# Kernel tuning notes

Measured on AMD Instinct MI355X. Metric: run time of the kernel, lower is better.

The kernel has to match this reference:

```python
import jax, jax.numpy as jnp
import numpy as np

N, C, H, W = 4, 128, 128, 128
G, K, PAD, DIL = 4, 3, 1, 1
P = K * K
HID = 4 * C
EPS = 1e-6


def ln(x, w, b):
    m = jnp.mean(x, -1, keepdims=True)
    v = jnp.mean((x - m) ** 2, -1, keepdims=True)
    return (x - m) * jax.lax.rsqrt(v + EPS) * w + b


def linear(x, w, b):
    return x @ w.T + b


def grid_sample_zeros(img, grid):
    # img: (B,Hi,Wi,Cc); grid: (B,L,P,2) xy in [-1,1]; bilinear, zeros padding, align_corners=False
    B, Hi, Wi, Cc = img.shape
    gx = (grid[..., 0] + 1.0) * (Wi * 0.5) - 0.5
    gy = (grid[..., 1] + 1.0) * (Hi * 0.5) - 0.5
    x0 = jnp.floor(gx)
    y0 = jnp.floor(gy)
    wx1 = gx - x0
    wy1 = gy - y0
    flat = img.reshape(B, Hi * Wi, Cc)
    Bq, L, Pq = gx.shape

    def tap(yy, xx, wgt):
        valid = (xx >= 0) & (xx <= Wi - 1) & (yy >= 0) & (yy <= Hi - 1)
        idx = (jnp.clip(yy, 0, Hi - 1) * Wi + jnp.clip(xx, 0, Wi - 1)).astype(jnp.int32)
        v = jnp.take_along_axis(flat, idx.reshape(B, L * Pq)[..., None], axis=1)
        return v.reshape(B, L, Pq, Cc) * (wgt * valid)[..., None]

    return (tap(y0, x0, (1 - wx1) * (1 - wy1))
            + tap(y0, x0 + 1, wx1 * (1 - wy1))
            + tap(y0 + 1, x0, (1 - wx1) * wy1)
            + tap(y0 + 1, x0 + 1, wx1 * wy1))


def dcn_core(x, offset, mask):
    # faithful port of dcnv3_core_pytorch (stride=1, offset_scale=1.0)
    n, h, w, c = x.shape
    gc = c // G
    xp = jnp.pad(x, ((0, 0), (PAD, PAD), (PAD, PAD), (0, 0)))
    hi, wi = h + 2 * PAD, w + 2 * PAD
    base = (DIL * (K - 1)) // 2 + 0.5
    ref_y = (base + jnp.arange(h, dtype=jnp.float32)) / hi
    ref_x = (base + jnp.arange(w, dtype=jnp.float32)) / wi
    ref = jnp.stack([jnp.broadcast_to(ref_x[None, :], (h, w)),
                     jnp.broadcast_to(ref_y[:, None], (h, w))], -1)  # (h,w,2) xy
    ks = jnp.arange(K, dtype=jnp.float32) * DIL - (DIL * (K - 1)) // 2
    gxk, gyk = jnp.meshgrid(ks, ks, indexing='ij')  # x slow, y fast (torch meshgrid order)
    grid = jnp.tile(jnp.stack([gxk / wi, gyk / hi], -1).reshape(P, 2), (G, 1))  # (G*P,2)
    sn = jnp.array([wi, hi], jnp.float32)
    loc = ref[None, :, :, None, :] + grid[None, None, None] + offset.reshape(n, h, w, G * P, 2) / sn
    sg = (2.0 * loc - 1.0).reshape(n, h * w, G, P, 2).transpose(0, 2, 1, 3, 4).reshape(n * G, h * w, P, 2)
    img = xp.reshape(n, hi, wi, G, gc).transpose(0, 3, 1, 2, 4).reshape(n * G, hi, wi, gc)
    samp = grid_sample_zeros(img, sg)  # (n*G, h*w, P, gc)
    m = mask.reshape(n, h * w, G, P).transpose(0, 2, 1, 3).reshape(n * G, h * w, P)
    out = jnp.einsum('blpc,blp->blc', samp, m)
    return out.reshape(n, G, h * w, gc).transpose(0, 2, 1, 3).reshape(n, h, w, c)


def dcn_forward(xcl, dw_w, dw_b, dwln_w, dwln_b, off_w, off_b, mask_w, mask_b, outproj_w, outproj_b):
    n, h, w, c = xcl.shape
    y = jax.lax.conv_general_dilated(xcl.transpose(0, 3, 1, 2), dw_w, (1, 1),
                                     ((PAD, PAD), (PAD, PAD)),
                                     dimension_numbers=('NCHW', 'OIHW', 'NCHW'),
                                     feature_group_count=C)
    y = y + dw_b[None, :, None, None]
    x1 = jax.nn.gelu(ln(y.transpose(0, 2, 3, 1), dwln_w, dwln_b), approximate=False)
    offset = linear(x1, off_w, off_b)
    m = jax.nn.softmax(linear(x1, mask_w, mask_b).reshape(n, h, w, G, P), -1).reshape(n, h, w, G * P)
    out = dcn_core(x1, offset, m)
    return linear(out, outproj_w, outproj_b)


def setup_inputs():
    key = jax.random.key(0)
    ks = jax.random.split(key, 8)
    s = 0.02
    return {
        "x": jax.random.normal(ks[0], (N, C, H, W), jnp.float32),
        "norm1_w": jnp.ones((C,), jnp.float32), "norm1_b": jnp.zeros((C,), jnp.float32),
        "dw_w": jax.random.normal(ks[1], (C, 1, K, K), jnp.float32) * 0.1,
        "dw_b": jnp.zeros((C,), jnp.float32),
        "dwln_w": jnp.ones((C,), jnp.float32), "dwln_b": jnp.zeros((C,), jnp.float32),
        "off_w": jax.random.normal(ks[2], (G * P * 2, C), jnp.float32) * 0.05,
        "off_b": jax.random.normal(ks[3], (G * P * 2,), jnp.float32) * 0.5,
        "mask_w": jax.random.normal(ks[4], (G * P, C), jnp.float32) * 0.05,
        "mask_b": jnp.zeros((G * P,), jnp.float32),
        "outproj_w": jax.random.normal(ks[5], (C, C), jnp.float32) * s,
        "outproj_b": jnp.zeros((C,), jnp.float32),
        "norm2_w": jnp.ones((C,), jnp.float32), "norm2_b": jnp.zeros((C,), jnp.float32),
        "fc1_w": jax.random.normal(ks[6], (HID, C), jnp.float32) * s,
        "fc1_b": jnp.zeros((HID,), jnp.float32),
        "fc2_w": jax.random.normal(ks[7], (C, HID), jnp.float32) * s,
        "fc2_b": jnp.zeros((C,), jnp.float32),
    }


def reference(x, norm1_w, norm1_b, dw_w, dw_b, dwln_w, dwln_b, off_w, off_b,
              mask_w, mask_b, outproj_w, outproj_b, norm2_w, norm2_b,
              fc1_w, fc1_b, fc2_w, fc2_b):
    # pre-norm branch (layer_scale=None, post_norm=False, res_post_norm=False, drop_path=Identity)
    xcl = ln(x.transpose(0, 2, 3, 1), norm1_w, norm1_b)  # channels_first -> channels_last LN
    d = dcn_forward(xcl, dw_w, dw_b, dwln_w, dwln_b, off_w, off_b, mask_w, mask_b, outproj_w, outproj_b)
    x = x + d.transpose(0, 3, 1, 2)
    y = ln(x.transpose(0, 2, 3, 1), norm2_w, norm2_b)
    y = linear(jax.nn.gelu(linear(y, fc1_w, fc1_b), approximate=False), fc2_w, fc2_b)
    return x + y.transpose(0, 3, 1, 2)
```

## Files before the change

### kernel.cpp

```cpp
#include <hip/hip_runtime.h>

typedef unsigned short ushort_t;
typedef short short8 __attribute__((ext_vector_type(8)));
typedef float f32x4 __attribute__((ext_vector_type(4)));
typedef ushort_t ushort8v __attribute__((ext_vector_type(8)));
typedef ushort_t ushort4v __attribute__((ext_vector_type(4)));

#define HWsz 16384
#define NHWsz 65536
#define YS 136

__device__ __forceinline__ float b2f(ushort_t u){ return __uint_as_float(((unsigned)u)<<16); }
__device__ __forceinline__ ushort_t f2b(float f){
  unsigned x = __float_as_uint(f);
  x += 0x7fffu + ((x>>16)&1u);
  return (ushort_t)(x>>16);
}
__device__ __forceinline__ float gelu_fast(float x){
  float t = x*x;
  float e = __expf(x*(1.5957691216f + 0.0713548163f*t));
  return x - x*__builtin_amdgcn_rcpf(1.0f + e);
}

#define XSW(p, b) ((p)*256 + ((b) ^ (((p)&7)<<4)))

__global__ __launch_bounds__(256) void kW_cvt(const float* __restrict__ w1, const float* __restrict__ w2,
    const float* __restrict__ offw, const float* __restrict__ maskw, const float* __restrict__ dww,
    const float* __restrict__ pw, const float* __restrict__ offb, const float* __restrict__ mb,
    ushort_t* __restrict__ w1b, ushort_t* __restrict__ w2b, ushort_t* __restrict__ owmb,
    float* __restrict__ dwwT, ushort_t* __restrict__ pwh, ushort_t* __restrict__ pwl,
    float* __restrict__ obm){
  int i = blockIdx.x*256 + threadIdx.x;
  w1b[i] = f2b(w1[i]);
  w2b[i] = f2b(w2[i]);
  if (i < 16384){
    int row = i >> 7, k = i & 127;
    float v = 0.f;
    if (row < 72) v = offw[row*128 + k];
    else if (row < 108) v = maskw[(row-72)*128 + k];
    owmb[i] = f2b(v);
    float pv = pw[i];
    ushort_t hi = f2b(pv);
    pwh[i] = hi;
    pwl[i] = f2b(pv - b2f(hi));
  }
  if (i < 1152){
    int k = i >> 7, c = i & 127;
    dwwT[i] = dww[c*9 + k];
  }
  if (i < 128){
    obm[i] = (i < 72) ? offb[i] : ((i < 108) ? mb[i-72] : 0.f);
  }
}

__global__ __launch_bounds__(256) void kA_ln1(const float* __restrict__ x,
    const float* __restrict__ w, const float* __restrict__ b,
    ushort_t* __restrict__ xcl){
  __shared__ float tile[128*66];
  __shared__ float psum[256], psq[256];
  __shared__ float ms[64], rs[64];
  int t = threadIdx.x;
  int pos0 = blockIdx.x * 64;
  int n = pos0 >> 14, hw0 = pos0 & 16383;
  const float* xb = x + (size_t)n*128*HWsz + hw0;
  for (int i=0;i<32;i++){
    int e = i*256+t;
    int c = e>>6, p = e&63;
    tile[c*66+p] = xb[(size_t)c*HWsz + p];
  }
  __syncthreads();
  {
    int part = t>>6, p = t&63;
    float s=0.f, q=0.f;
    for (int c=part*32; c<part*32+32; c++){ float v = tile[c*66+p]; s+=v; q+=v*v; }
    psum[part*64+p]=s; psq[part*64+p]=q;
  }
  __syncthreads();
  if (t<64){
    float s=psum[t]+psum[64+t]+psum[128+t]+psum[192+t];
    float q=psq[t]+psq[64+t]+psq[128+t]+psq[192+t];
    float m = s*(1.0f/128.0f);
    float v = q*(1.0f/128.0f)-m*m;
    ms[t]=m; rs[t]=rsqrtf(v+1e-6f);
  }
  __syncthreads();
  for (int i=0;i<32;i++){
    int e = i*256+t;
    int p = e>>7, c = e&127;
    float v = (tile[c*66+p]-ms[p])*rs[p]*w[c]+b[c];
    xcl[(size_t)(pos0+p)*128 + c] = f2b(v);
  }
}

__global__ __launch_bounds__(256) void kB_dw(const ushort_t* __restrict__ xcl,
    const float* __restrict__ dwwT, const float* __restrict__ dwb,
    const float* __restrict__ lnw, const float* __restrict__ lnb,
    ushort_t* __restrict__ x1){
  __shared__ float partS[16*17], partQ[16*17];
  __shared__ float ms[16], rs[16];
  int t = threadIdx.x;
  int pos0 = blockIdx.x*16;
  int n = pos0>>14, hw0 = pos0&16383, h = hw0>>7, w0 = hw0&127;
  int pp = t>>4, l = t&15, ch0 = l*8;
  int w = w0 + pp;
  float acc[8];
  {
    float4 b0 = *(const float4*)(dwb + ch0);
    float4 b1 = *(const float4*)(dwb + ch0 + 4);
    acc[0]=b0.x; acc[1]=b0.y; acc[2]=b0.z; acc[3]=b0.w;
    acc[4]=b1.x; acc[5]=b1.y; acc[6]=b1.z; acc[7]=b1.w;
  }
  #pragma unroll
  for (int kh=0; kh<3; kh++){
    int hy = h + kh - 1;
    if ((unsigned)hy < 128u){
      #pragma unroll
      for (int kw=0; kw<3; kw++){
        int wx = w + kw - 1;
        if ((unsigned)wx < 128u){
          ushort8v xv = *(const ushort8v*)(xcl + ((size_t)(n*16384 + hy*128 + wx))*128 + ch0);
          const float* wr = dwwT + (kh*3+kw)*128 + ch0;
          float4 w0v = *(const float4*)(wr);
          float4 w1v = *(const float4*)(wr+4);
          acc[0] += b2f(xv[0])*w0v.x; acc[1] += b2f(xv[1])*w0v.y;
          acc[2] += b2f(xv[2])*w0v.z; acc[3] += b2f(xv[3])*w0v.w;
          acc[4] += b2f(xv[4])*w1v.x; acc[5] += b2f(xv[5])*w1v.y;
          acc[6] += b2f(xv[6])*w1v.z; acc[7] += b2f(xv[7])*w1v.w;
        }
      }
    }
  }
  {
    float s=0.f, q=0.f;
    #pragma unroll
    for (int j=0;j<8;j++){ s+=acc[j]; q+=acc[j]*acc[j]; }
    partS[pp*17+l]=s; partQ[pp*17+l]=q;
  }
  __syncthreads();
  {
    int p = t>>4, j = t&15;
    float s = partS[p*17+j];
    float q = partQ[p*17+j];
    s += __shfl_xor(s, 1);  q += __shfl_xor(q, 1);
    s += __shfl_xor(s, 2);  q += __shfl_xor(q, 2);
    s += __shfl_xor(s, 4);  q += __shfl_xor(q, 4);
    s += __shfl_xor(s, 8);  q += __shfl_xor(q, 8);
    if (j == 0){
      float m = s*(1.0f/128.0f);
      float var = q*(1.0f/128.0f) - m*m;
      ms[p]=m; rs[p]=rsqrtf(var+1e-6f);
    }
  }
  __syncthreads();
  {
    float m = ms[pp], r = rs[pp];
    float4 lw0 = *(const float4*)(lnw + ch0);
    float4 lw1 = *(const float4*)(lnw + ch0 + 4);
    float4 lb0 = *(const float4*)(lnb + ch0);
    float4 lb1 = *(const float4*)(lnb + ch0 + 4);
    float lw[8] = {lw0.x,lw0.y,lw0.z,lw0.w,lw1.x,lw1.y,lw1.z,lw1.w};
    float lb[8] = {lb0.x,lb0.y,lb0.z,lb0.w,lb1.x,lb1.y,lb1.z,lb1.w};
    ushort8v o;
    #pragma unroll
    for (int j=0;j<8;j++){
      float v = (acc[j]-m)*r*lw[j]+lb[j];
      o[j] = f2b(gelu_fast(v));
    }
    *(ushort8v*)(x1 + (size_t)(pos0+pp)*128 + ch0) = o;
  }
}

#define RS 120
__global__ __launch_bounds__(256) void kCD_dcn(const ushort_t* __restrict__ x1,
    const ushort_t* __restrict__ owmb, const float* __restrict__ obm,
    ushort_t* __restrict__ dcnout){
  __shared__ __align__(16) ushort_t xLb[16*YS];
  __shared__ float raw[16*RS];
  __shared__ __align__(16) float descW[576*4];
  __shared__ __align__(16) int   descO[576*4];
  int t = threadIdx.x;
  int pos0 = blockIdx.x*16;
  int n = pos0>>14, hw0 = pos0&16383, h = hw0>>7, w0 = hw0&127;
  const size_t imgbase = (size_t)n*16384*128;

  *(ushort8v*)(xLb + (t>>4)*YS + (t&15)*8) = *(const ushort8v*)(x1 + (size_t)pos0*128 + t*8);
  __syncthreads();

  {
    int wave = t>>6, lane = t&63;
    int ma = lane&15, quad = lane>>4;
    short8 afrag[4];
    #pragma unroll
    for (int ks=0; ks<4; ks++)
      afrag[ks] = *(const short8*)(xLb + ma*YS + ks*32 + quad*8);
    f32x4 acc[2];
    acc[0] = (f32x4){0.f,0.f,0.f,0.f};
    acc[1] = (f32x4){0.f,0.f,0.f,0.f};
    #pragma unroll
    for (int tile=0; tile<2; tile++){
      const ushort_t* brow = owmb + (size_t)(wave*32 + tile*16 + ma)*128 + quad*8;
      #pragma unroll
      for (int ks=0; ks<4; ks++){
        short8 bfrag = *(const short8*)(brow + ks*32);
        acc[tile] = __builtin_amdgcn_mfma_f32_16x16x32_bf16(bfrag, afrag[ks], acc[tile], 0,0,0);
      }
    }
    #pragma unroll
    for (int tile=0; tile<2; tile++){
      int row0 = wave*32 + tile*16 + quad*4;
      if (row0 < 112){
        f32x4 bias4 = *(const f32x4*)(obm + row0);
        f32x4 o;
        #pragma unroll
        for (int r=0;r<4;r++) o[r] = acc[tile][r] + bias4[r];
        *(f32x4*)(raw + ma*RS + row0) = o;
      }
    }
  }
  __syncthreads();

  if (t < 64){
    int p = t>>2, g = t&3;
    float* mr = raw + p*RS + 72 + g*9;
    float mx = -1e30f;
    for (int q=0;q<9;q++) mx = fmaxf(mx, mr[q]);
    float e[9]; float ssum=0.f;
    for (int q=0;q<9;q++){ e[q]=expf(mr[q]-mx); ssum+=e[q]; }
    float inv = 1.0f/ssum;
    for (int q=0;q<9;q++) mr[q] = e[q]*inv;
  }
  __syncthreads();

  for (int it=0; it<3; it++){
    int tid = t + 256*it;
    if (tid < 576){
      int pp = tid/36, rem = tid - pp*36;
      int g = rem/9, p = rem - g*9;
      int i = p/3, j = p - i*3;
      float ox = raw[pp*RS + 2*(g*9+p)];
      float oy = raw[pp*RS + 2*(g*9+p)+1];
      float mval = raw[pp*RS + 72 + g*9 + p];
      float px = (float)(w0 + pp + i - 1) + ox;
      float py = (float)(h + j - 1) + oy;
      float fx0 = floorf(px), fy0 = floorf(py);
      int ix0 = (int)fx0, iy0 = (int)fy0;
      float fx = px - fx0, fy = py - fy0;
      float vx0 = ((unsigned)ix0     < 128u) ? 1.f : 0.f;
      float vx1 = ((unsigned)(ix0+1) < 128u) ? 1.f : 0.f;
      float vy0 = ((unsigned)iy0     < 128u) ? 1.f : 0.f;
      float vy1 = ((unsigned)(iy0+1) < 128u) ? 1.f : 0.f;
      int cx0 = min(max(ix0,0),127), cx1 = min(max(ix0+1,0),127);
      int cy0 = min(max(iy0,0),127), cy1 = min(max(iy0+1,0),127);
      float4 wv;
      wv.x = (1.f-fx)*(1.f-fy)*mval*vx0*vy0;
      wv.y = fx*(1.f-fy)*mval*vx1*vy0;
      wv.z = (1.f-fx)*fy*mval*vx0*vy1;
      wv.w = fx*fy*mval*vx1*vy1;
      int4 ov;
      ov.x = (cy0*128+cx0)*128;
      ov.y = (cy0*128+cx1)*128;
      ov.z = (cy1*128+cx0)*128;
      ov.w = (cy1*128+cx1)*128;
      *(float4*)(descW + tid*4) = wv;
      *(int4*)(descO + tid*4) = ov;
    }
  }
  __syncthreads();

  {
    int pp = t>>4, l = t&15;
    int ch0 = l*8, g = l>>2;
    const ushort_t* ib = x1 + imgbase + ch0;
    float acc[8];
    #pragma unroll
    for (int j=0;j<8;j++) acc[j]=0.f;
    int dbase = pp*36 + g*9;
    #pragma unroll
    for (int p=0;p<9;p++){
      float4 wv = *(const float4*)(descW + (dbase+p)*4);
      int4  ov = *(const int4*)(descO + (dbase+p)*4);
      ushort8v v00 = *(const ushort8v*)(ib + ov.x);
      ushort8v v10 = *(const ushort8v*)(ib + ov.y);
      ushort8v v01 = *(const ushort8v*)(ib + ov.z);
      ushort8v v11 = *(const ushort8v*)(ib + ov.w);
      #pragma unroll
      for (int j=0;j<8;j++){
        float s = wv.x*b2f(v00[j]) + wv.y*b2f(v10[j]) + wv.z*b2f(v01[j]) + wv.w*b2f(v11[j]);
        acc[j] += s;
      }
    }
    ushort8v outv;
    #pragma unroll
    for (int j=0;j<8;j++) outv[j] = f2b(acc[j]);
    *(ushort8v*)(dcnout + (size_t)(pos0+pp)*128 + ch0) = outv;
  }
}

__global__ __launch_bounds__(256) void kEFG(const ushort_t* __restrict__ dcnout,
    const ushort_t* __restrict__ pwh, const ushort_t* __restrict__ pwl,
    const float* __restrict__ pb, const float* __restrict__ x,
    const float* __restrict__ n2w, const float* __restrict__ n2b,
    const ushort_t* __restrict__ w1b, const float* __restrict__ b1,
    const ushort_t* __restrict__ w2b, const float* __restrict__ b2,
    float* __restrict__ out){
  __shared__ __align__(16) char dxn[64*256];
  __shared__ __align__(16) char hidb[64*256];
  float* partS = (float*)hidb;
  float* partQ = partS + 64*17;
  float* msh   = partQ + 64*17;
  float* rsh   = msh + 64;

  int t = threadIdx.x;
  int pos0 = blockIdx.x*64;
  int n = pos0>>14, hw0 = pos0&16383;
  int wave = t>>6, lane = t&63;
  int ma = lane&15, quad = lane>>4;

  #pragma unroll
  for (int i=0;i<4;i++){
    int e = i*256 + t;
    int row = e>>4, c16 = e&15;
    ushort8v v = *(const ushort8v*)(dcnout + (size_t)pos0*128 + (size_t)e*8);
    *(ushort8v*)(dxn + XSW(row, c16*16)) = v;
  }
  __syncthreads();

  f32x4 acc[2][4];
  #pragma unroll
  for (int i=0;i<2;i++)
    #pragma unroll
    for (int mt=0; mt<4; mt++) acc[i][mt] = (f32x4){0.f,0.f,0.f,0.f};
  #pragma unroll
  for (int tile=0; tile<2; tile++){
    int c0 = wave*32 + tile*16;
    const ushort_t* bh = pwh + (size_t)(c0 + ma)*128 + quad*8;
    const ushort_t* bl = pwl + (size_t)(c0 + ma)*128 + quad*8;
    short8 bfh[4], bfl[4];
    #pragma unroll
    for (int ks=0; ks<4; ks++){
      bfh[ks] = *(const short8*)(bh + ks*32);
      bfl[ks] = *(const short8*)(bl + ks*32);
    }
    #pragma unroll
    for (int mt=0; mt<4; mt++){
      short8 a[4];
      #pragma unroll
      for (int ks=0; ks<4; ks++)
        a[ks] = *(const short8*)(dxn + XSW(mt*16+ma, ks*64 + quad*16));
      #pragma unroll
      for (int ks=0; ks<4; ks++){
        acc[tile][mt] = __builtin_amdgcn_mfma_f32_16x16x32_bf16(bfh[ks], a[ks], acc[tile][mt], 0,0,0);
        acc[tile][mt] = __builtin_amdgcn_mfma_f32_16x16x32_bf16(bfl[ks], a[ks], acc[tile][mt], 0,0,0);
      }
    }
  }

  ushort4v vbp[2][4];
  float sAcc[4], qAcc[4];
  #pragma unroll
  for (int mt=0; mt<4; mt++){ sAcc[mt]=0.f; qAcc[mt]=0.f; }
  #pragma unroll
  for (int tile=0; tile<2; tile++){
    int c0 = wave*32 + tile*16 + quad*4;
    f32x4 bias4 = *(const f32x4*)(pb + c0);
    #pragma unroll
    for (int mt=0; mt<4; mt++){
      int p = mt*16 + ma;
      ushort4v ov;
      #pragma unroll
      for (int r=0;r<4;r++){
        float res = x[((size_t)(n*128) + c0 + r)*HWsz + hw0 + p];
        float v = acc[tile][mt][r] + bias4[r] + res;
        ushort_t ub = f2b(v);
        ov[r] = ub;
        float vv = b2f(ub);
        sAcc[mt] += vv; qAcc[mt] += vv*vv;
      }
      vbp[tile][mt] = ov;
    }
  }
  #pragma unroll
  for (int mt=0; mt<4; mt++){
    int p = mt*16 + ma;
    partS[p*17 + wave*4 + quad] = sAcc[mt];
    partQ[p*17 + wave*4 + quad] = qAcc[mt];
  }
  __syncthreads();
  {
    int p = t>>2, j = t&3;
    float s = partS[p*17+4*j] + partS[p*17+4*j+1] + partS[p*17+4*j+2] + partS[p*17+4*j+3];
    float q = partQ[p*17+4*j] + partQ[p*17+4*j+1] + partQ[p*17+4*j+2] + partQ[p*17+4*j+3];
    s += __shfl_xor(s, 1);  q += __shfl_xor(q, 1);
    s += __shfl_xor(s, 2);  q += __shfl_xor(q, 2);
    if (j == 0){
      float m = s*(1.0f/128.0f);
      float var = q*(1.0f/128.0f) - m*m;
      msh[p] = m; rsh[p] = rsqrtf(var+1e-6f);
    }
  }
  __syncthreads();

  #pragma unroll
  for (int tile=0; tile<2; tile++){
    int c0 = wave*32 + tile*16 + quad*4;
    f32x4 w4 = *(const f32x4*)(n2w + c0);
    f32x4 b4 = *(const f32x4*)(n2b + c0);
    #pragma unroll
    for (int mt=0; mt<4; mt++){
      int p = mt*16 + ma;
      float m = msh[p], r = rsh[p];
      ushort4v nv;
      #pragma unroll
      for (int rr=0;rr<4;rr++) nv[rr] = f2b((b2f(vbp[tile][mt][rr])-m)*r*w4[rr] + b4[rr]);
      *(ushort4v*)(dxn + XSW(p, c0*2)) = nv;
    }
  }
  __syncthreads();

  f32x4 acc2[2][4];
  #pragma unroll
  for (int i=0;i<2;i++)
    #pragma unroll
    for (int mt=0; mt<4; mt++) acc2[i][mt] = (f32x4){0.f,0.f,0.f,0.f};

  #pragma unroll
  for (int nc=0; nc<4; nc++){
    #pragma unroll
    for (int tt=0; tt<2; tt++){
      int n0g = nc*128 + wave*32 + tt*16;
      const ushort_t* brow = w1b + (size_t)(n0g + ma)*128 + quad*8;
      short8 bf[4];
      #pragma unroll
      for (int ks=0; ks<4; ks++) bf[ks] = *(const short8*)(brow + ks*32);
      int n0 = n0g + quad*4;
      f32x4 bias4 = *(const f32x4*)(b1 + n0);
      int nloc = wave*32 + tt*16 + quad*4;
      #pragma unroll
      for (int mt=0; mt<4; mt++){
        short8 a[4];
        #pragma unroll
        for (int ks=0; ks<4; ks++)
          a[ks] = *(const short8*)(dxn + XSW(mt*16+ma, ks*64 + quad*16));
        f32x4 a0 = (f32x4){0.f,0.f,0.f,0.f};
        #pragma unroll
        for (int ks=0; ks<4; ks++)
          a0 = __builtin_amdgcn_mfma_f32_16x16x32_bf16(bf[ks], a[ks], a0, 0,0,0);
        ushort4v hv;
        #pragma unroll
        for (int r=0;r<4;r++) hv[r] = f2b(gelu_fast(a0[r] + bias4[r]));
        *(ushort4v*)(hidb + XSW(mt*16+ma, nloc*2)) = hv;
      }
    }
    __syncthreads();

    #pragma unroll
    for (int ksl=0; ksl<4; ksl++){
      int kk = nc*128 + ksl*32;
      short8 wc0 = *(const short8*)(w2b + (size_t)(wave*32 + ma)*512 + kk + quad*8);
      short8 wc1 = *(const short8*)(w2b + (size_t)(wave*32 + 16 + ma)*512 + kk + quad*8);
      #pragma unroll
      for (int mt=0; mt<4; mt++){
        short8 hc = *(const short8*)(hidb + XSW(mt*16+ma, ksl*64 + quad*16));
        acc2[0][mt] = __builtin_amdgcn_mfma_f32_16x16x32_bf16(wc0, hc, acc2[0][mt], 0,0,0);
        acc2[1][mt] = __builtin_amdgcn_mfma_f32_16x16x32_bf16(wc1, hc, acc2[1][mt], 0,0,0);
      }
    }
    if (nc < 3) __syncthreads();
  }

  #pragma unroll
  for (int tile=0; tile<2; tile++){
    int c0 = wave*32 + tile*16 + quad*4;
    f32x4 bias4 = *(const f32x4*)(b2 + c0);
    #pragma unroll
    for (int mt=0; mt<4; mt++){
      int p = mt*16 + ma;
      #pragma unroll
      for (int r=0;r<4;r++){
        float v = acc2[tile][mt][r] + bias4[r] + b2f(vbp[tile][mt][r]);
        out[((size_t)(n*128) + c0 + r)*HWsz + hw0 + p] = v;
      }
    }
  }
}

extern "C" void kernel_launch(void* const* d_in, const int* in_sizes, int n_in,
                              void* d_out, int out_size, void* d_ws, size_t ws_size,
                              hipStream_t stream){
  const float* x     = (const float*)d_in[0];
  const float* n1w   = (const float*)d_in[1];
  const float* n1b   = (const float*)d_in[2];
  const float* dww   = (const float*)d_in[3];
  const float* dwb   = (const float*)d_in[4];
  const float* dwlnw = (const float*)d_in[5];
  const float* dwlnb = (const float*)d_in[6];
  const float* offw  = (const float*)d_in[7];
  const float* offb  = (const float*)d_in[8];
  const float* maskw = (const float*)d_in[9];
  const float* maskb = (const float*)d_in[10];
  const float* pw    = (const float*)d_in[11];
  const float* pb    = (const float*)d_in[12];
  const float* n2w   = (const float*)d_in[13];
  const float* n2b   = (const float*)d_in[14];
  const float* w1    = (const float*)d_in[15];
  const float* b1    = (const float*)d_in[16];
  const float* w2    = (const float*)d_in[17];
  const float* b2    = (const float*)d_in[18];

  char* wsb = (char*)d_ws;
  ushort_t* R0   = (ushort_t*)(wsb);
  ushort_t* R1   = (ushort_t*)(wsb + (16u<<20));
  ushort_t* w1b  = (ushort_t*)(wsb + (32u<<20));
  ushort_t* w2b  = (ushort_t*)(wsb + (32u<<20) + (128u<<10));
  ushort_t* owmb = (ushort_t*)(wsb + (32u<<20) + (256u<<10));
  ushort_t* pwh  = (ushort_t*)(wsb + (32u<<20) + (288u<<10));
  ushort_t* pwl  = (ushort_t*)(wsb + (32u<<20) + (320u<<10));
  float*    dwwT = (float*)(wsb + (32u<<20) + (352u<<10));
  float*    obm  = (float*)(wsb + (32u<<20) + (358u<<10));
  float* out = (float*)d_out;

  hipLaunchKernelGGL(kW_cvt,  dim3(256),   dim3(256), 0, stream, w1, w2, offw, maskw, dww, pw, offb, maskb, w1b, w2b, owmb, dwwT, pwh, pwl, obm);
  hipLaunchKernelGGL(kA_ln1,  dim3(1024),  dim3(256), 0, stream, x, n1w, n1b, R0);
  hipLaunchKernelGGL(kB_dw,   dim3(4096),  dim3(256), 0, stream, R0, dwwT, dwb, dwlnw, dwlnb, R1);
  hipLaunchKernelGGL(kCD_dcn, dim3(4096),  dim3(256), 0, stream, R1, owmb, obm, R0);
  hipLaunchKernelGGL(kEFG,    dim3(1024),  dim3(256), 0, stream, R0, pwh, pwl, pb, x, n2w, n2b, w1b, b1, w2b, b2, out);
}
```

Measured before the change: 250.7 us.

## Double kEFG position tile to 128 and shrink hidden chunk to 64

The fused outproj+LN2+MLP kernel now handles 128 positions per block instead of 64, so each weight fragment loaded from global memory is reused across twice as many rows. The hidden dimension is processed in 8 chunks of 64 with a narrower swizzled hidden buffer, and the LN2 reduction now uses wave shuffles before a smaller shared-memory pass. The cost is more accumulator registers per thread, which can lower occupancy or cause spills, and half as many blocks (512) on the GPU.

```diff
diff --git a/kernel.cpp b/kernel.cpp
--- a/kernel.cpp
+++ b/kernel.cpp
@@ -23,6 +23,7 @@
 }
 
 #define XSW(p, b) ((p)*256 + ((b) ^ (((p)&7)<<4)))
+#define HS2(p, b) ((p)*128 + ((b) ^ (((p)&7)<<4)))
 
 __global__ __launch_bounds__(256) void kW_cvt(const float* __restrict__ w1, const float* __restrict__ w2,
     const float* __restrict__ offw, const float* __restrict__ maskw, const float* __restrict__ dww,
@@ -303,21 +304,21 @@
     const ushort_t* __restrict__ w1b, const float* __restrict__ b1,
     const ushort_t* __restrict__ w2b, const float* __restrict__ b2,
     float* __restrict__ out){
-  __shared__ __align__(16) char dxn[64*256];
-  __shared__ __align__(16) char hidb[64*256];
+  __shared__ __align__(16) char dxn[128*256];
+  __shared__ __align__(16) char hidb[128*128];
   float* partS = (float*)hidb;
-  float* partQ = partS + 64*17;
-  float* msh   = partQ + 64*17;
-  float* rsh   = msh + 64;
+  float* partQ = partS + 128*5;
+  float* msh   = partQ + 128*5;
+  float* rsh   = msh + 128;
 
   int t = threadIdx.x;
-  int pos0 = blockIdx.x*64;
+  int pos0 = blockIdx.x*128;
   int n = pos0>>14, hw0 = pos0&16383;
   int wave = t>>6, lane = t&63;
   int ma = lane&15, quad = lane>>4;
 
   #pragma unroll
-  for (int i=0;i<4;i++){
+  for (int i=0;i<8;i++){
     int e = i*256 + t;
     int row = e>>4, c16 = e&15;
     ushort8v v = *(const ushort8v*)(dcnout + (size_t)pos0*128 + (size_t)e*8);
@@ -325,11 +326,11 @@
   }
   __syncthreads();
 
-  f32x4 acc[2][4];
+  f32x4 acc[2][8];
   #pragma unroll
   for (int i=0;i<2;i++)
     #pragma unroll
-    for (int mt=0; mt<4; mt++) acc[i][mt] = (f32x4){0.f,0.f,0.f,0.f};
+    for (int mt=0; mt<8; mt++) acc[i][mt] = (f32x4){0.f,0.f,0.f,0.f};
   #pragma unroll
   for (int tile=0; tile<2; tile++){
     int c0 = wave*32 + tile*16;
@@ -342,7 +343,7 @@
       bfl[ks] = *(const short8*)(bl + ks*32);
     }
     #pragma unroll
-    for (int mt=0; mt<4; mt++){
+    for (int mt=0; mt<8; mt++){
       short8 a[4];
       #pragma unroll
       for (int ks=0; ks<4; ks++)
@@ -355,16 +356,16 @@
     }
   }
 
-  ushort4v vbp[2][4];
-  float sAcc[4], qAcc[4];
-  #pragma unroll
-  for (int mt=0; mt<4; mt++){ sAcc[mt]=0.f; qAcc[mt]=0.f; }
+  ushort4v vbp[2][8];
+  float sAcc[8], qAcc[8];
+  #pragma unroll
+  for (int mt=0; mt<8; mt++){ sAcc[mt]=0.f; qAcc[mt]=0.f; }
   #pragma unroll
   for (int tile=0; tile<2; tile++){
     int c0 = wave*32 + tile*16 + quad*4;
     f32x4 bias4 = *(const f32x4*)(pb + c0);
     #pragma unroll
-    for (int mt=0; mt<4; mt++){
+    for (int mt=0; mt<8; mt++){
       int p = mt*16 + ma;
       ushort4v ov;
       #pragma unroll
@@ -380,23 +381,28 @@
     }
   }
   #pragma unroll
-  for (int mt=0; mt<4; mt++){
-    int p = mt*16 + ma;
-    partS[p*17 + wave*4 + quad] = sAcc[mt];
-    partQ[p*17 + wave*4 + quad] = qAcc[mt];
-  }
-  __syncthreads();
-  {
-    int p = t>>2, j = t&3;
-    float s = partS[p*17+4*j] + partS[p*17+4*j+1] + partS[p*17+4*j+2] + partS[p*17+4*j+3];
-    float q = partQ[p*17+4*j] + partQ[p*17+4*j+1] + partQ[p*17+4*j+2] + partQ[p*17+4*j+3];
-    s += __shfl_xor(s, 1);  q += __shfl_xor(q, 1);
-    s += __shfl_xor(s, 2);  q += __shfl_xor(q, 2);
-    if (j == 0){
-      float m = s*(1.0f/128.0f);
-      float var = q*(1.0f/128.0f) - m*m;
-      msh[p] = m; rsh[p] = rsqrtf(var+1e-6f);
-    }
+  for (int mt=0; mt<8; mt++){
+    float s = sAcc[mt], q = qAcc[mt];
+    s += __shfl_xor(s, 16);  q += __shfl_xor(q, 16);
+    s += __shfl_xor(s, 32);  q += __shfl_xor(q, 32);
+    sAcc[mt] = s; qAcc[mt] = q;
+  }
+  if (quad == 0){
+    #pragma unroll
+    for (int mt=0; mt<8; mt++){
+      int p = mt*16 + ma;
+      partS[p*5 + wave] = sAcc[mt];
+      partQ[p*5 + wave] = qAcc[mt];
+    }
+  }
+  __syncthreads();
+  if (t < 128){
+    int p = t;
+    float s = partS[p*5+0] + partS[p*5+1] + partS[p*5+2] + partS[p*5+3];
+    float q = partQ[p*5+0] + partQ[p*5+1] + partQ[p*5+2] + partQ[p*5+3];
+    float m = s*(1.0f/128.0f);
+    float var = q*(1.0f/128.0f) - m*m;
+    msh[p] = m; rsh[p] = rsqrtf(var+1e-6f);
   }
   __syncthreads();
 
@@ -406,7 +412,7 @@
     f32x4 w4 = *(const f32x4*)(n2w + c0);
     f32x4 b4 = *(const f32x4*)(n2b + c0);
     #pragma unroll
-    for (int mt=0; mt<4; mt++){
+    for (int mt=0; mt<8; mt++){
       int p = mt*16 + ma;
       float m = msh[p], r = rsh[p];
       ushort4v nv;
@@ -417,26 +423,23 @@
   }
   __syncthreads();
 
-  f32x4 acc2[2][4];
+  f32x4 acc2[2][8];
   #pragma unroll
   for (int i=0;i<2;i++)
     #pragma unroll
-    for (int mt=0; mt<4; mt++) acc2[i][mt] = (f32x4){0.f,0.f,0.f,0.f};
-
-  #pragma unroll
-  for (int nc=0; nc<4; nc++){
-    #pragma unroll
-    for (int tt=0; tt<2; tt++){
-      int n0g = nc*128 + wave*32 + tt*16;
+    for (int mt=0; mt<8; mt++) acc2[i][mt] = (f32x4){0.f,0.f,0.f,0.f};
+
+  for (int nc=0; nc<8; nc++){
+    {
+      int n0g = nc*64 + wave*16;
       const ushort_t* brow = w1b + (size_t)(n0g + ma)*128 + quad*8;
       short8 bf[4];
       #pragma unroll
       for (int ks=0; ks<4; ks++) bf[ks] = *(const short8*)(brow + ks*32);
-      int n0 = n0g + quad*4;
-      f32x4 bias4 = *(const f32x4*)(b1 + n0);
-      int nloc = wave*32 + tt*16 + quad*4;
-      #pragma unroll
-      for (int mt=0; mt<4; mt++){
+      f32x4 bias4 = *(const f32x4*)(b1 + n0g + quad*4);
+      int nloc = wave*16 + quad*4;
+      #pragma unroll
+      for (int mt=0; mt<8; mt++){
         short8 a[4];
         #pragma unroll
         for (int ks=0; ks<4; ks++)
@@ -448,24 +451,24 @@
         ushort4v hv;
         #pragma unroll
         for (int r=0;r<4;r++) hv[r] = f2b(gelu_fast(a0[r] + bias4[r]));
-        *(ushort4v*)(hidb + XSW(mt*16+ma, nloc*2)) = hv;
+        *(ushort4v*)(hidb + HS2(mt*16+ma, nloc*2)) = hv;
       }
     }
     __syncthreads();
 
     #pragma unroll
-    for (int ksl=0; ksl<4; ksl++){
-      int kk = nc*128 + ksl*32;
+    for (int ksl=0; ksl<2; ksl++){
+      int kk = nc*64 + ksl*32;
       short8 wc0 = *(const short8*)(w2b + (size_t)(wave*32 + ma)*512 + kk + quad*8);
       short8 wc1 = *(const short8*)(w2b + (size_t)(wave*32 + 16 + ma)*512 + kk + quad*8);
       #pragma unroll
-      for (int mt=0; mt<4; mt++){
-        short8 hc = *(const short8*)(hidb + XSW(mt*16+ma, ksl*64 + quad*16));
+      for (int mt=0; mt<8; mt++){
+        short8 hc = *(const short8*)(hidb + HS2(mt*16+ma, ksl*64 + quad*16));
         acc2[0][mt] = __builtin_amdgcn_mfma_f32_16x16x32_bf16(wc0, hc, acc2[0][mt], 0,0,0);
         acc2[1][mt] = __builtin_amdgcn_mfma_f32_16x16x32_bf16(wc1, hc, acc2[1][mt], 0,0,0);
       }
     }
-    if (nc < 3) __syncthreads();
+    if (nc < 7) __syncthreads();
   }
 
   #pragma unroll
@@ -473,7 +476,7 @@
     int c0 = wave*32 + tile*16 + quad*4;
     f32x4 bias4 = *(const f32x4*)(b2 + c0);
     #pragma unroll
-    for (int mt=0; mt<4; mt++){
+    for (int mt=0; mt<8; mt++){
       int p = mt*16 + ma;
       #pragma unroll
       for (int r=0;r<4;r++){
@@ -523,5 +526,5 @@
   hipLaunchKernelGGL(kA_ln1,  dim3(1024),  dim3(256), 0, stream, x, n1w, n1b, R0);
   hipLaunchKernelGGL(kB_dw,   dim3(4096),  dim3(256), 0, stream, R0, dwwT, dwb, dwlnw, dwlnb, R1);
   hipLaunchKernelGGL(kCD_dcn, dim3(4096),  dim3(256), 0, stream, R1, owmb, obm, R0);
-  hipLaunchKernelGGL(kEFG,    dim3(1024),  dim3(256), 0, stream, R0, pwh, pwl, pb, x, n2w, n2b, w1b, b1, w2b, b2, out);
-}
+  hipLaunchKernelGGL(kEFG,    dim3(512),   dim3(256), 0, stream, R0, pwh, pwl, pb, x, n2w, n2b, w1b, b1, w2b, b2, out);
+}
```

After: 259.1 us. 1.03x slower.
